# Kernel tuning notes

Measured on AMD Instinct MI355X. Metric: run time of the kernel, lower is better.

Reference implementation:

```python
import math
import jax
import jax.numpy as jnp
import numpy as np

KS = 7  # kernel_size


def _make_cdt_kernel():
    # kornia.create_meshgrid(k,k,normalized=False) -> coords; centered; hypot -> exp(d/-0.35)
    r = np.arange(KS, dtype=np.float32) - (KS // 2)
    yy, xx = np.meshgrid(r, r, indexing="ij")
    k = np.exp(np.hypot(xx, yy) / -0.35)
    return jnp.asarray(k, jnp.float32)[None, None]  # (1,1,KS,KS) OIHW


def setup_inputs() -> dict:
    key = jax.random.key(0)
    B, C, H, W = 32, 3, 256, 256
    u = jax.random.uniform(key, (B, C, H, W), dtype=jnp.float32)
    image = (u < 0.005).astype(jnp.float32)
    return {"image": image}


def reference(image):
    B, C, H, W = image.shape
    kernel = _make_cdt_kernel()
    n_iters = math.ceil(max(H, W) / (KS // 2))  # static
    x = image.reshape(B * C, 1, H, W)
    out0 = jnp.zeros_like(x)

    def step(carry, i):
        out, boundary = carry
        conv = jax.lax.conv_general_dilated(
            boundary, kernel, (1, 1), "SAME",
            dimension_numbers=("NCHW", "OIHW", "NCHW"))
        # -0.35*log(conv) with posinf (conv==0) replaced by 0, exactly as
        # torch.nan_to_num(cdt, posinf=0.0); safe-log form avoids inf/nan.
        pos = conv > 0
        cdt = jnp.where(pos, -0.35 * jnp.log(jnp.where(pos, conv, 1.0)), 0.0)
        mask = cdt > 0
        offset = i.astype(jnp.float32) * (KS / 2)  # i * kernel_size / 2 (true div)
        out = out + jnp.where(mask, offset + cdt, 0.0)
        boundary = jnp.where(mask, 1.0, boundary)
        return (out, boundary), None

    (out, _), _ = jax.lax.scan(step, (out0, x), jnp.arange(n_iters))
    return out.reshape(B, C, H, W)
```

## Files before the change

### kernel.cpp

```cpp
#include <hip/hip_runtime.h>


typedef unsigned short u16x4 __attribute__((ext_vector_type(4)));
typedef unsigned int u32x2 __attribute__((ext_vector_type(2)));
typedef union { u16x4 v; unsigned int d[2]; } U16U;

#define BIGV (1 << 20)
#define GUARD 12
#define ROWB ((GUARD + 256 + GUARD) * 2)
#define CHB (256 * ROWB)

__global__ __launch_bounds__(256) void k_rowdist(const float* __restrict__ img,
                                                 unsigned char* __restrict__ d1) {
  const int lane = threadIdx.x & 63;
  const int wv = threadIdx.x >> 6;
  const int row = blockIdx.x * 4 + wv;
  const int x0 = lane * 4;

  const float4 v = *reinterpret_cast<const float4*>(&img[(size_t)row * 256 + x0]);

  int c0 = (v.x != 0.0f) ? -x0 : BIGV;
  int c1 = (v.y != 0.0f) ? -(x0 + 1) : BIGV;
  int c2 = (v.z != 0.0f) ? -(x0 + 2) : BIGV;
  int c3 = (v.w != 0.0f) ? -(x0 + 3) : BIGV;
  const int p0 = c0;
  const int p1 = min(c1, p0);
  const int p2 = min(c2, p1);
  const int p3 = min(c3, p2);
  int incl = p3;
#pragma unroll
  for (int off = 1; off < 64; off <<= 1) {
    int o = __shfl_up(incl, off, 64);
    if (lane >= off) incl = min(incl, o);
  }
  int excl = __shfl_up(incl, 1, 64);
  if (lane == 0) excl = BIGV;
  const int df0 = x0 + min(p0, excl);
  const int df1 = x0 + 1 + min(p1, excl);
  const int df2 = x0 + 2 + min(p2, excl);
  const int df3 = x0 + 3 + min(p3, excl);

  int g0 = (v.x != 0.0f) ? x0 : BIGV;
  int g1 = (v.y != 0.0f) ? (x0 + 1) : BIGV;
  int g2 = (v.z != 0.0f) ? (x0 + 2) : BIGV;
  int g3 = (v.w != 0.0f) ? (x0 + 3) : BIGV;
  const int q3 = g3;
  const int q2 = min(g2, q3);
  const int q1 = min(g1, q2);
  const int q0 = min(g0, q1);
  int incl2 = q0;
#pragma unroll
  for (int off = 1; off < 64; off <<= 1) {
    int o = __shfl_down(incl2, off, 64);
    if (lane < 64 - off) incl2 = min(incl2, o);
  }
  int excl2 = __shfl_down(incl2, 1, 64);
  if (lane == 63) excl2 = BIGV;
  const int db0 = min(q0, excl2) - x0;
  const int db1 = min(q1, excl2) - (x0 + 1);
  const int db2 = min(q2, excl2) - (x0 + 2);
  const int db3 = min(q3, excl2) - (x0 + 3);

  const unsigned int d0 = (unsigned int)min(min(df0, db0), 127);
  const unsigned int d1v = (unsigned int)min(min(df1, db1), 127);
  const unsigned int d2 = (unsigned int)min(min(df2, db2), 127);
  const unsigned int d3 = (unsigned int)min(min(df3, db3), 127);
  const int ch = row >> 8, y = row & 255;
  const size_t base = (size_t)ch * CHB + (size_t)y * ROWB;

  u32x2 pk;
  pk.x = d0 | (d1v << 16);
  pk.y = d2 | (d3 << 16);
  *reinterpret_cast<u32x2*>(&d1[base + 2 * GUARD + 2 * x0]) = pk;

  u32x2 gv;
  gv.x = 0x007F007Fu;
  gv.y = 0x007F007Fu;
  if (lane < 3)
    *reinterpret_cast<u32x2*>(&d1[base + lane * 8]) = gv;
  else if (lane >= 61)
    *reinterpret_cast<u32x2*>(&d1[base + 536 + (lane - 61) * 8]) = gv;
}

#define TAPROW(s_, t_, A0, A1, A2, A3, A4, A5, A6)                              \
  do {                                                                          \
    const unsigned int r0_ = R[(s_) + (t_)][0];                                 \
    const unsigned int r1_ = R[(s_) + (t_)][1];                                 \
    const unsigned int r2_ = R[(s_) + (t_)][2];                                 \
    A0 += (((__builtin_amdgcn_alignbyte(r1_, r0_, 1) + Cp) & 0x80808080u) >> 7);\
    A1 += (((__builtin_amdgcn_alignbyte(r1_, r0_, 2) + Cp) & 0x80808080u) >> 7);\
    A2 += (((__builtin_amdgcn_alignbyte(r1_, r0_, 3) + Cp) & 0x80808080u) >> 7);\
    A3 += (((r1_ + Cp) & 0x80808080u) >> 7);                                    \
    A4 += (((__builtin_amdgcn_alignbyte(r2_, r1_, 1) + Cp) & 0x80808080u) >> 7);\
    A5 += (((__builtin_amdgcn_alignbyte(r2_, r1_, 2) + Cp) & 0x80808080u) >> 7);\
    A6 += (((__builtin_amdgcn_alignbyte(r2_, r1_, 3) + Cp) & 0x80808080u) >> 7);\
  } while (0)

#define TAPROWC(s_, t_, A0, A1, A2, A4, A5, A6)   \
  do {                                                                          \
    const unsigned int r0_ = R[(s_) + (t_)][0];                                 \
    const unsigned int r1_ = R[(s_) + (t_)][1];                                 \
    const unsigned int r2_ = R[(s_) + (t_)][2];                                 \
    A0 += (((__builtin_amdgcn_alignbyte(r1_, r0_, 1) + Cp) & 0x80808080u) >> 7);\
    A1 += (((__builtin_amdgcn_alignbyte(r1_, r0_, 2) + Cp) & 0x80808080u) >> 7);\
    A2 += (((__builtin_amdgcn_alignbyte(r1_, r0_, 3) + Cp) & 0x80808080u) >> 7);\
    A4 += (((__builtin_amdgcn_alignbyte(r2_, r1_, 1) + Cp) & 0x80808080u) >> 7);\
    A5 += (((__builtin_amdgcn_alignbyte(r2_, r1_, 2) + Cp) & 0x80808080u) >> 7);\
    A6 += (((__builtin_amdgcn_alignbyte(r2_, r1_, 3) + Cp) & 0x80808080u) >> 7);\
  } while (0)

#define EPI(s_)                                                                 \
  do {                                                                          \
    const unsigned int Dc = R[(s_) + 3][1];                                     \
    U16U u_;                                                                    \
    u_.d[0] = __builtin_amdgcn_perm(0u, Dc, 0x0C010C00u);                       \
    u_.d[1] = __builtin_amdgcn_perm(0u, Dc, 0x0C030C02u);                       \
    const u16x4 V = __builtin_elementwise_max(u_.v, kOne);                      \
    const u16x4 I16 = ((V - kOne) * k86) >> k8;       \
    U16U ci_, ii_;                                                              \
    ii_.v = I16;                                                                \
    ci_.v = k127 - (u16x4)(I16 + I16 + I16);                                    \
    const unsigned int Cp =                                                     \
        __builtin_amdgcn_perm(ci_.d[1], ci_.d[0], 0x06040200u);                 \
    unsigned int aA = 0, aB = 0, aC = 0, aD = 0;                                \
    TAPROW(s_, 0, aD, aD, aC, aC, aC, aD, aD);                                  \
    TAPROW(s_, 1, aD, aC, aB, aB, aB, aC, aD);                                  \
    TAPROW(s_, 2, aC, aB, aA, aA, aA, aB, aC);                                  \
    TAPROWC(s_, 3, aC, aB, aA, aA, aB, aC);                                     \
    TAPROW(s_, 4, aC, aB, aA, aA, aA, aB, aC);                                  \
    TAPROW(s_, 5, aD, aC, aB, aB, aB, aC, aD);                                  \
    TAPROW(s_, 6, aD, aD, aC, aC, aC, aD, aD);                                  \
    float4 res4;                                                                \
    float* rp = &res4.x;                                                        \
    const unsigned int iw0 = ii_.d[0], iw1 = ii_.d[1];                          \
    _Pragma("unroll") for (int k = 0; k < 4; ++k) {                             \
      const float fa = (float)((aA >> (8 * k)) & 255u);                         \
      const float fb = (float)((aB >> (8 * k)) & 255u);                         \
      const float fc = (float)((aC >> (8 * k)) & 255u);                         \
      const float fd = (float)((aD >> (8 * k)) & 255u);                         \
      const float conv =                                                        \
          W4 - (fa * wA + fb * wB + fc * wC + fd * wD);                         \
      const unsigned int ik = (k < 2) ? ((iw0 >> (16 * k)) & 0xFFFFu)           \
                                      : ((iw1 >> (16 * (k - 2))) & 0xFFFFu);    \
      const unsigned int dk = (Dc >> (8 * k)) & 255u;                           \
      const float r =                                                           \
          fmaf(3.5f, (float)ik, -0.35f * __logf(fmaxf(conv, 1e-30f)));          \
      rp[k] = (dk > 0u && conv > 1e-6f) ? r : 0.0f;                             \
    }                                                                           \
    *reinterpret_cast<float4*>(&out[obase + (size_t)(r0 + (s_)) * 256]) = res4; \
  } while (0)

__global__ __launch_bounds__(256, 4) void k_fused(const unsigned char* __restrict__ d1,
                                                  float* __restrict__ out) {
  const int ch = blockIdx.y;
  const int xt = blockIdx.x;
  const int x0 = xt * 32;
  const int tid = threadIdx.x;
  const int lastxt = (int)gridDim.x - 1;

  __shared__ __align__(16) unsigned char s1[256 * 80];
  __shared__ __align__(16) unsigned char Ds[262 * 44];

  const unsigned char* src = d1 + (size_t)ch * CHB + 2 * x0 + 2 * (GUARD - 4);
#pragma unroll
  for (int it = 0; it < 5; ++it) {
    const int idx = it * 256 + tid;
    const int y = (idx * 13108) >> 16;
    const int seg = idx - y * 5;
    *reinterpret_cast<uint4*>(&s1[y * 80 + seg * 16]) =
        *reinterpret_cast<const uint4*>(&src[y * ROWB + seg * 16]);
  }
  if (tid < 66) {
    const int r = (tid * 5958) >> 16;
    const int c = tid - r * 11;
    const int row = (r < 3) ? r : r + 256;
    *reinterpret_cast<unsigned int*>(&Ds[row * 44 + c * 4]) = 0x7F7F7F7Fu;
  }
  __syncthreads();

  const int ybot = 255 * 80;
#pragma unroll 1
  for (int it = 0; it < 10; ++it) {
    const int idx = it * 256 + tid;
    const int y = (idx * 6554) >> 16;
    const int g = idx - y * 10;
    const bool ghost = (xt == 0 && g == 0) || (xt == lastxt && g == 9);
    if (ghost) {
      *reinterpret_cast<unsigned int*>(&Ds[(y + 3) * 44 + g * 4]) = 0x7F7F7F7Fu;
      continue;
    }
    const int g8 = g * 8;
    const int rb = y * 80 + g8;
    u16x4 b = *reinterpret_cast<const u16x4*>(&s1[rb]);
    int au = rb, ad = rb;
#pragma unroll
    for (int k = 1; k <= 8; ++k) {
      au = max(au - 80, g8);
      ad = min(ad + 80, ybot + g8);
      const u16x4 u = *reinterpret_cast<const u16x4*>(&s1[au]);
      const u16x4 w = *reinterpret_cast<const u16x4*>(&s1[ad]);
      const unsigned short ks = (unsigned short)k;
      const u16x4 kk = {ks, ks, ks, ks};
      b = __builtin_elementwise_min(b, __builtin_elementwise_max(u, kk));
      b = __builtin_elementwise_min(b, __builtin_elementwise_max(w, kk));
    }
    int bm = max(max((int)b.x, (int)b.y), max((int)b.z, (int)b.w));
    int k = 9;
    while (k < bm) {
#pragma unroll
      for (int j = 0; j < 4; ++j) {
        const unsigned short ks = (unsigned short)(k + j);
        au = max(au - 80, g8);
        ad = min(ad + 80, ybot + g8);
        const u16x4 u = *reinterpret_cast<const u16x4*>(&s1[au]);
        const u16x4 w = *reinterpret_cast<const u16x4*>(&s1[ad]);
        const u16x4 kk = {ks, ks, ks, ks};
        b = __builtin_elementwise_min(b, __builtin_elementwise_max(u, kk));
        b = __builtin_elementwise_min(b, __builtin_elementwise_max(w, kk));
      }
      k += 4;
      bm = max(max((int)b.x, (int)b.y), max((int)b.z, (int)b.w));
    }
    union { u16x4 v; u32x2 d; } cc;
    cc.v = b;
    const unsigned int packed = __builtin_amdgcn_perm(cc.d.y, cc.d.x, 0x06040200u);
    *reinterpret_cast<unsigned int*>(&Ds[(y + 3) * 44 + g * 4]) = packed;
  }
  __syncthreads();

  const float wA = 3.17814e-2f, wB = 2.35426e-3f, wC = 1.91126e-4f, wD = 1.35150e-5f;
  const float W4 = 8.0f * wA + 12.0f * wB + 16.0f * wC + 12.0f * wD;
  const u16x4 kOne = {1, 1, 1, 1};
  const u16x4 k86 = {86, 86, 86, 86};
  const u16x4 k8 = {8, 8, 8, 8};
  const u16x4 k127 = {127, 127, 127, 127};

  const int cg = tid & 7;
  const int rg = tid >> 3;
  const int r0 = rg * 8;
  const int jb = cg * 4;
  const size_t obase = (size_t)ch * 65536 + x0 + cg * 4;

  unsigned int R[14][3];
#pragma unroll
  for (int u = 0; u < 14; ++u) {
    const unsigned char* p = &Ds[(r0 + u) * 44 + jb];
    R[u][0] = *reinterpret_cast<const unsigned int*>(p);
    R[u][1] = *reinterpret_cast<const unsigned int*>(p + 4);
    R[u][2] = *reinterpret_cast<const unsigned int*>(p + 8);
  }

  EPI(0); EPI(1); EPI(2); EPI(3); EPI(4); EPI(5); EPI(6); EPI(7);
}

extern "C" void kernel_launch(void* const* d_in, const int* in_sizes, int n_in,
                              void* d_out, int out_size, void* d_ws, size_t ws_size,
                              hipStream_t stream) {
  const float* img = (const float*)d_in[0];
  float* out = (float*)d_out;
  unsigned char* Dbuf = (unsigned char*)d_ws;

  const int total = in_sizes[0];
  const int nch = total >> 16;

  k_rowdist<<<dim3(nch * 64), dim3(256), 0, stream>>>(img, Dbuf);
  k_fused<<<dim3(8, nch), dim3(256), 0, stream>>>(Dbuf, out);
}
```

Before: 46.26 us.

## Split fused kernel into two vertical row tiles per channel for more blocks

The fused kernel now tiles each channel into two 128-row halves, doubling the grid to 8x2xnch. Each block computes the column distance for only its 134 rows (with a 3-row halo) and emits 4 output rows per thread instead of 8, which cuts the register array and the Ds shared buffer. Launch bounds are raised to request 6 blocks per CU. Each block still loads the full 256-row column slice into shared memory, so global-to-LDS traffic for s1 doubles in exchange for more parallelism and occupancy.

```diff
diff --git a/kernel.cpp b/kernel.cpp
--- a/kernel.cpp
+++ b/kernel.cpp
@@ -147,19 +147,21 @@
           fmaf(3.5f, (float)ik, -0.35f * __logf(fmaxf(conv, 1e-30f)));          \
       rp[k] = (dk > 0u && conv > 1e-6f) ? r : 0.0f;                             \
     }                                                                           \
-    *reinterpret_cast<float4*>(&out[obase + (size_t)(r0 + (s_)) * 256]) = res4; \
+    *reinterpret_cast<float4*>(&out[obase + (size_t)(s_) * 256]) = res4;        \
   } while (0)
 
-__global__ __launch_bounds__(256, 4) void k_fused(const unsigned char* __restrict__ d1,
+__global__ __launch_bounds__(256, 6) void k_fused(const unsigned char* __restrict__ d1,
                                                   float* __restrict__ out) {
-  const int ch = blockIdx.y;
+  const int ch = blockIdx.z;
+  const int yt = blockIdx.y;
   const int xt = blockIdx.x;
   const int x0 = xt * 32;
+  const int y0 = yt * 128;
   const int tid = threadIdx.x;
   const int lastxt = (int)gridDim.x - 1;
 
   __shared__ __align__(16) unsigned char s1[256 * 80];
-  __shared__ __align__(16) unsigned char Ds[262 * 44];
+  __shared__ __align__(16) unsigned char Ds[134 * 44];
 
   const unsigned char* src = d1 + (size_t)ch * CHB + 2 * x0 + 2 * (GUARD - 4);
 #pragma unroll
@@ -170,23 +172,20 @@
     *reinterpret_cast<uint4*>(&s1[y * 80 + seg * 16]) =
         *reinterpret_cast<const uint4*>(&src[y * ROWB + seg * 16]);
   }
-  if (tid < 66) {
-    const int r = (tid * 5958) >> 16;
-    const int c = tid - r * 11;
-    const int row = (r < 3) ? r : r + 256;
-    *reinterpret_cast<unsigned int*>(&Ds[row * 44 + c * 4]) = 0x7F7F7F7Fu;
-  }
   __syncthreads();
 
   const int ybot = 255 * 80;
 #pragma unroll 1
-  for (int it = 0; it < 10; ++it) {
+  for (int it = 0; it < 6; ++it) {
     const int idx = it * 256 + tid;
-    const int y = (idx * 6554) >> 16;
-    const int g = idx - y * 10;
-    const bool ghost = (xt == 0 && g == 0) || (xt == lastxt && g == 9);
+    if (idx >= 1340) break;
+    const int r = (idx * 6554) >> 16;
+    const int g = idx - r * 10;
+    const int y = y0 + r - 3;
+    const bool ghost =
+        (xt == 0 && g == 0) || (xt == lastxt && g == 9) || y < 0 || y > 255;
     if (ghost) {
-      *reinterpret_cast<unsigned int*>(&Ds[(y + 3) * 44 + g * 4]) = 0x7F7F7F7Fu;
+      *reinterpret_cast<unsigned int*>(&Ds[r * 44 + g * 4]) = 0x7F7F7F7Fu;
       continue;
     }
     const int g8 = g * 8;
@@ -224,7 +223,7 @@
     union { u16x4 v; u32x2 d; } cc;
     cc.v = b;
     const unsigned int packed = __builtin_amdgcn_perm(cc.d.y, cc.d.x, 0x06040200u);
-    *reinterpret_cast<unsigned int*>(&Ds[(y + 3) * 44 + g * 4]) = packed;
+    *reinterpret_cast<unsigned int*>(&Ds[r * 44 + g * 4]) = packed;
   }
   __syncthreads();
 
@@ -237,20 +236,20 @@
 
   const int cg = tid & 7;
   const int rg = tid >> 3;
-  const int r0 = rg * 8;
+  const int rl0 = rg * 4;
   const int jb = cg * 4;
-  const size_t obase = (size_t)ch * 65536 + x0 + cg * 4;
-
-  unsigned int R[14][3];
-#pragma unroll
-  for (int u = 0; u < 14; ++u) {
-    const unsigned char* p = &Ds[(r0 + u) * 44 + jb];
+  const size_t obase = (size_t)ch * 65536 + (size_t)(y0 + rl0) * 256 + x0 + cg * 4;
+
+  unsigned int R[10][3];
+#pragma unroll
+  for (int u = 0; u < 10; ++u) {
+    const unsigned char* p = &Ds[(rl0 + u) * 44 + jb];
     R[u][0] = *reinterpret_cast<const unsigned int*>(p);
     R[u][1] = *reinterpret_cast<const unsigned int*>(p + 4);
     R[u][2] = *reinterpret_cast<const unsigned int*>(p + 8);
   }
 
-  EPI(0); EPI(1); EPI(2); EPI(3); EPI(4); EPI(5); EPI(6); EPI(7);
+  EPI(0); EPI(1); EPI(2); EPI(3);
 }
 
 extern "C" void kernel_launch(void* const* d_in, const int* in_sizes, int n_in,
@@ -264,5 +263,5 @@
   const int nch = total >> 16;
 
   k_rowdist<<<dim3(nch * 64), dim3(256), 0, stream>>>(img, Dbuf);
-  k_fused<<<dim3(8, nch), dim3(256), 0, stream>>>(Dbuf, out);
+  k_fused<<<dim3(8, 2, nch), dim3(256), 0, stream>>>(Dbuf, out);
 }
```

Measured after the change: 45.80 us. No clear change (-1.0%).
